# Performance work log

Hardware: AMD Instinct MI355X
Metric: run time of the kernel (lower is better)

## Reference

```python
import jax, jax.numpy as jnp
import numpy as np

N_NODES = 100000


def _gcn_layer(x, src, dst, W, b, n_nodes):
    # x: [N, Cin]; src/dst already include self-loops
    h = x @ W  # [N, Cout]
    deg = jax.ops.segment_sum(jnp.ones_like(dst, dtype=h.dtype), dst,
                              num_segments=n_nodes)  # in-degree incl. self-loop
    dinv = jnp.where(deg > 0, deg ** -0.5, 0.0)
    norm = dinv[src] * dinv[dst]  # [E]
    msg = h[src] * norm[:, None]  # [E, Cout]
    out = jax.ops.segment_sum(msg, dst, num_segments=n_nodes)
    return out + b


def setup_inputs() -> dict:
    key = jax.random.key(0)
    k1, k2, k3, k4, k5, k6, k7 = jax.random.split(key, 7)
    E = 6400000
    x = jax.random.normal(k1, (N_NODES, 5), dtype=jnp.float32)
    edge_index = jax.random.randint(k2, (2, E), 0, N_NODES, dtype=jnp.int64)
    edge_f = jax.random.normal(k3, (E,), dtype=jnp.float32)
    edge_attr = jax.random.normal(k4, (E, 1), dtype=jnp.float32)
    # GCNConv params (glorot-ish scale)
    W1 = jax.random.normal(k5, (5, 8), dtype=jnp.float32) * (1.0 / np.sqrt(5))
    b1 = jnp.zeros((8,), dtype=jnp.float32)
    W2 = jax.random.normal(k6, (8, 5), dtype=jnp.float32) * (1.0 / np.sqrt(8))
    b2 = jnp.zeros((5,), dtype=jnp.float32)
    return {"x": x, "edge_index": edge_index, "edge_f": edge_f,
            "edge_attr": edge_attr, "W1": W1, "b1": b1, "W2": W2, "b2": b2}


def reference(x, edge_index, edge_f, edge_attr, W1, b1, W2, b2):
    n = x.shape[0]
    loops = jnp.arange(n, dtype=edge_index.dtype)
    src = jnp.concatenate([edge_index[0], loops])  # add self-loops (PyG default)
    dst = jnp.concatenate([edge_index[1], loops])
    h = _gcn_layer(x, src, dst, W1, b1, n)
    h = _gcn_layer(h, src, dst, W2, b2, n)
    return h
```

## Files before the change

### kernel.cpp

```cpp
#include <hip/hip_runtime.h>
#include <hip/hip_fp16.h>


#define TPB 256
#define VPB 256
#define B_BITS 8
#define MAXB 512
#define CAP 17408
#define NBLK_E 512
#define EPB 12500
#define SCT 512
#define DGT 512

typedef int int4e __attribute__((ext_vector_type(4)));
typedef _Float16 h8 __attribute__((ext_vector_type(8)));

__device__ __forceinline__ int4e ntload4(const int* p) {
    return __builtin_nontemporal_load((const int4e*)p);
}
__device__ __forceinline__ int ntload(const int* p) {
    return __builtin_nontemporal_load(p);
}

__global__ void k_init(int B, int* __restrict__ bpos) {
    int b = blockIdx.x * blockDim.x + threadIdx.x;
    if (b < B) bpos[b] = b * CAP;
}

__global__ __launch_bounds__(SCT) void k_scat(const int* __restrict__ src,
        const int* __restrict__ dst, int E, int B,
        int* __restrict__ bpos, int* __restrict__ pairs) {
    __shared__ int sorted[EPB];
    __shared__ int hist[MAXB], scn[MAXB], cur[MAXB], gbase[MAXB];
    int t = threadIdx.x;
    for (int i = t; i < MAXB; i += SCT) hist[i] = 0;
    __syncthreads();
    int lo = blockIdx.x * EPB;
    int n = min(E - lo, EPB);
    int n4 = n & ~3;
    for (int i = t * 4; i < n4; i += SCT * 4) {
        int4e d4 = ntload4(dst + lo + i);
        atomicAdd(&hist[d4.x >> B_BITS], 1);
        atomicAdd(&hist[d4.y >> B_BITS], 1);
        atomicAdd(&hist[d4.z >> B_BITS], 1);
        atomicAdd(&hist[d4.w >> B_BITS], 1);
    }
    for (int i = n4 + t; i < n; i += SCT)
        atomicAdd(&hist[dst[lo + i] >> B_BITS], 1);
    __syncthreads();
    if (t < MAXB) scn[t] = hist[t];
    __syncthreads();
    for (int off = 1; off < MAXB; off <<= 1) {
        int v = (t >= off && t < MAXB) ? scn[t - off] : 0;
        __syncthreads();
        if (t < MAXB) scn[t] += v;
        __syncthreads();
    }
    if (t < MAXB) {
        int h = hist[t];
        cur[t] = scn[t] - h;
        gbase[t] = (t < B && h) ? atomicAdd(&bpos[t], h) : 0;
    }
    __syncthreads();
    for (int i = t * 4; i < n4; i += SCT * 4) {
        int4e d4 = ntload4(dst + lo + i);
        int4e s4 = ntload4(src + lo + i);
        int p;
        p = atomicAdd(&cur[d4.x >> B_BITS], 1); sorted[p] = (s4.x << B_BITS) | (d4.x & (VPB - 1));
        p = atomicAdd(&cur[d4.y >> B_BITS], 1); sorted[p] = (s4.y << B_BITS) | (d4.y & (VPB - 1));
        p = atomicAdd(&cur[d4.z >> B_BITS], 1); sorted[p] = (s4.z << B_BITS) | (d4.z & (VPB - 1));
        p = atomicAdd(&cur[d4.w >> B_BITS], 1); sorted[p] = (s4.w << B_BITS) | (d4.w & (VPB - 1));
    }
    for (int i = n4 + t; i < n; i += SCT) {
        int d = dst[lo + i], s = src[lo + i];
        int p = atomicAdd(&cur[d >> B_BITS], 1);
        sorted[p] = (s << B_BITS) | (d & (VPB - 1));
    }
    __syncthreads();
    int wave = t >> 6, lane = t & 63;
    for (int b2 = wave; b2 < B; b2 += (SCT >> 6)) {
        int h = hist[b2];
        int st = scn[b2] - h;
        int gb = gbase[b2];
        for (int j = lane; j < h; j += 64)
            pairs[gb + j] = sorted[st + j];
    }
}

__global__ __launch_bounds__(DGT) void k_degxs(const int* __restrict__ pairs,
        const int* __restrict__ bpos, int N,
        const float* __restrict__ x,
        unsigned int* __restrict__ jinfo, _Float16* __restrict__ xs) {
    __shared__ int hist[VPB];
    __shared__ int scn[VPB];
    int t = threadIdx.x, b = blockIdx.x;
    if (t < VPB) hist[t] = 0;
    __syncthreads();
    int base = b * CAP;
    int n = bpos[b] - base, n4 = n & ~3;
    for (int i = t * 4; i < n4; i += DGT * 4) {
        int4e p = ntload4(pairs + base + i);
        atomicAdd(&hist[p.x & (VPB - 1)], 1);
        atomicAdd(&hist[p.y & (VPB - 1)], 1);
        atomicAdd(&hist[p.z & (VPB - 1)], 1);
        atomicAdd(&hist[p.w & (VPB - 1)], 1);
    }
    for (int i = n4 + t; i < n; i += DGT)
        atomicAdd(&hist[pairs[base + i] & (VPB - 1)], 1);
    __syncthreads();
    if (t < VPB) scn[t] = hist[t];
    __syncthreads();
    for (int off = 1; off < VPB; off <<= 1) {
        int v = (t >= off && t < VPB) ? scn[t - off] : 0;
        __syncthreads();
        if (t < VPB) scn[t] += v;
        __syncthreads();
    }
    int node = b * VPB + t;
    if (t < VPB && node < N) {
        int h = hist[t];
        int start = base + scn[t] - h;
        jinfo[node] = ((unsigned int)start << 9) | (unsigned int)h;
        float di = rsqrtf((float)(h + 1));
        const float* xp = x + (size_t)node * 5;
        h8 v;
        v[0] = (_Float16)(xp[0] * di); v[1] = (_Float16)(xp[1] * di);
        v[2] = (_Float16)(xp[2] * di); v[3] = (_Float16)(xp[3] * di);
        v[4] = (_Float16)(xp[4] * di);
        v[5] = (_Float16)0.f; v[6] = (_Float16)0.f; v[7] = (_Float16)0.f;
        *(h8*)(xs + (size_t)node * 8) = v;
    }
}

__global__ __launch_bounds__(1024) void k_agg1(const int* __restrict__ pairs_,
        const int* __restrict__ bpos, const unsigned int* __restrict__ jinfo,
        const _Float16* __restrict__ xs, const float* __restrict__ b1,
        const float* __restrict__ W1, const float* __restrict__ W2,
        _Float16* __restrict__ h2s, int N) {
    __shared__ int csr[CAP];
    __shared__ int js[VPB], ct[VPB], cur[VPB];
    int* pairs = (int*)pairs_;
    int t = threadIdx.x, b = blockIdx.x;
    int base = b * CAP;
    if (t < VPB) {
        int node = b * VPB + t;
        int s = 0, c = 0;
        if (node < N) {
            unsigned int u = jinfo[node];
            s = (int)(u >> 9) - base;
            c = (int)(u & 511u);
        }
        js[t] = s; ct[t] = c; cur[t] = s;
    }
    __syncthreads();
    int n = bpos[b] - base, n4 = n & ~3;
    for (int i = t * 4; i < n4; i += 1024 * 4) {
        int4e p = ntload4(pairs + base + i);
        int q;
        q = atomicAdd(&cur[p.x & (VPB - 1)], 1); csr[q] = p.x >> B_BITS;
        q = atomicAdd(&cur[p.y & (VPB - 1)], 1); csr[q] = p.y >> B_BITS;
        q = atomicAdd(&cur[p.z & (VPB - 1)], 1); csr[q] = p.z >> B_BITS;
        q = atomicAdd(&cur[p.w & (VPB - 1)], 1); csr[q] = p.w >> B_BITS;
    }
    for (int i = n4 + t; i < n; i += 1024) {
        int p = pairs[base + i];
        int q = atomicAdd(&cur[p & (VPB - 1)], 1);
        csr[q] = p >> B_BITS;
    }
    __syncthreads();
    for (int i = t; i < n; i += 1024)
        __builtin_nontemporal_store(csr[i], pairs + base + i);
    int lane = t & 3, ln = t >> 2;
    int node = b * VPB + ln;
    if (node >= N) return;
    int s0 = js[ln], cn = ct[ln];
    float a0 = 0.f, a1 = 0.f, a2 = 0.f, a3 = 0.f, a4 = 0.f;
    int j = lane;
    for (; j + 12 < cn; j += 16) {
        int sA = csr[s0 + j];
        int sB = csr[s0 + j + 4];
        int sC = csr[s0 + j + 8];
        int sD = csr[s0 + j + 12];
        h8 vA = *(const h8*)(xs + (size_t)sA * 8);
        h8 vB = *(const h8*)(xs + (size_t)sB * 8);
        h8 vC = *(const h8*)(xs + (size_t)sC * 8);
        h8 vD = *(const h8*)(xs + (size_t)sD * 8);
        a0 += (float)vA[0] + (float)vB[0] + (float)vC[0] + (float)vD[0];
        a1 += (float)vA[1] + (float)vB[1] + (float)vC[1] + (float)vD[1];
        a2 += (float)vA[2] + (float)vB[2] + (float)vC[2] + (float)vD[2];
        a3 += (float)vA[3] + (float)vB[3] + (float)vC[3] + (float)vD[3];
        a4 += (float)vA[4] + (float)vB[4] + (float)vC[4] + (float)vD[4];
    }
    for (; j < cn; j += 4) {
        int sA = csr[s0 + j];
        h8 vA = *(const h8*)(xs + (size_t)sA * 8);
        a0 += (float)vA[0]; a1 += (float)vA[1]; a2 += (float)vA[2];
        a3 += (float)vA[3]; a4 += (float)vA[4];
    }
#pragma unroll
    for (int d = 1; d < 4; d <<= 1) {
        a0 += __shfl_xor(a0, d); a1 += __shfl_xor(a1, d);
        a2 += __shfl_xor(a2, d); a3 += __shfl_xor(a3, d);
        a4 += __shfl_xor(a4, d);
    }
    h8 sv = *(const h8*)(xs + (size_t)node * 8);
    float tc[5];
    tc[0] = a0 + (float)sv[0]; tc[1] = a1 + (float)sv[1];
    tc[2] = a2 + (float)sv[2]; tc[3] = a3 + (float)sv[3];
    tc[4] = a4 + (float)sv[4];
    float di = rsqrtf((float)(cn + 1));
    float o1[8];
#pragma unroll
    for (int jj = 0; jj < 8; ++jj) {
        float h = 0.f;
#pragma unroll
        for (int c = 0; c < 5; ++c) h += tc[c] * W1[c * 8 + jj];
        o1[jj] = h * di + b1[jj];
    }
    if (lane == 0) {
        float hv[5];
#pragma unroll
        for (int k = 0; k < 5; ++k) {
            float h = 0.f;
#pragma unroll
            for (int jj = 0; jj < 8; ++jj) h += o1[jj] * W2[jj * 5 + k];
            hv[k] = h * di;
        }
        h8 w;
        w[0] = (_Float16)hv[0]; w[1] = (_Float16)hv[1]; w[2] = (_Float16)hv[2];
        w[3] = (_Float16)hv[3]; w[4] = (_Float16)hv[4];
        w[5] = (_Float16)0.f; w[6] = (_Float16)0.f; w[7] = (_Float16)0.f;
        *(h8*)(h2s + (size_t)node * 8) = w;
    }
}

__global__ __launch_bounds__(TPB) void k_agg2(const int* __restrict__ pairs,
        const unsigned int* __restrict__ jinfo, const _Float16* __restrict__ h2s,
        const float* __restrict__ b2, float* __restrict__ out, int N) {
    int gid = blockIdx.x * blockDim.x + threadIdx.x;
    int node = gid >> 3, lane = gid & 7;
    if (node >= N) return;
    unsigned int u = jinfo[node];
    int jsa = (int)(u >> 9), cn = (int)(u & 511u);
    float a0 = 0.f, a1 = 0.f, a2 = 0.f, a3 = 0.f, a4 = 0.f;
    int j = lane;
    for (; j + 24 < cn; j += 32) {
        int sA = ntload(pairs + jsa + j);
        int sB = ntload(pairs + jsa + j + 8);
        int sC = ntload(pairs + jsa + j + 16);
        int sD = ntload(pairs + jsa + j + 24);
        h8 vA = *(const h8*)(h2s + (size_t)sA * 8);
        h8 vB = *(const h8*)(h2s + (size_t)sB * 8);
        h8 vC = *(const h8*)(h2s + (size_t)sC * 8);
        h8 vD = *(const h8*)(h2s + (size_t)sD * 8);
        a0 += (float)vA[0] + (float)vB[0] + (float)vC[0] + (float)vD[0];
        a1 += (float)vA[1] + (float)vB[1] + (float)vC[1] + (float)vD[1];
        a2 += (float)vA[2] + (float)vB[2] + (float)vC[2] + (float)vD[2];
        a3 += (float)vA[3] + (float)vB[3] + (float)vC[3] + (float)vD[3];
        a4 += (float)vA[4] + (float)vB[4] + (float)vC[4] + (float)vD[4];
    }
    for (; j < cn; j += 8) {
        int sA = ntload(pairs + jsa + j);
        h8 vA = *(const h8*)(h2s + (size_t)sA * 8);
        a0 += (float)vA[0]; a1 += (float)vA[1]; a2 += (float)vA[2];
        a3 += (float)vA[3]; a4 += (float)vA[4];
    }
#pragma unroll
    for (int d = 1; d < 8; d <<= 1) {
        a0 += __shfl_xor(a0, d); a1 += __shfl_xor(a1, d);
        a2 += __shfl_xor(a2, d); a3 += __shfl_xor(a3, d);
        a4 += __shfl_xor(a4, d);
    }
    if (lane == 0) {
        float di = rsqrtf((float)(cn + 1));
        h8 sv = *(const h8*)(h2s + (size_t)node * 8);
        float* op = out + (size_t)node * 5;
        op[0] = (a0 + (float)sv[0]) * di + b2[0];
        op[1] = (a1 + (float)sv[1]) * di + b2[1];
        op[2] = (a2 + (float)sv[2]) * di + b2[2];
        op[3] = (a3 + (float)sv[3]) * di + b2[3];
        op[4] = (a4 + (float)sv[4]) * di + b2[4];
    }
}

extern "C" void kernel_launch(void* const* d_in, const int* in_sizes, int n_in,
                              void* d_out, int out_size, void* d_ws, size_t ws_size,
                              hipStream_t stream) {
    const float* x   = (const float*)d_in[0];
    const int*  eidx = (const int*)d_in[1];
    const float* W1 = (const float*)d_in[4];
    const float* b1 = (const float*)d_in[5];
    const float* W2 = (const float*)d_in[6];
    const float* b2 = (const float*)d_in[7];
    float* out = (float*)d_out;

    const int N = in_sizes[0] / 5;
    const int E = in_sizes[1] / 2;
    const int* src = eidx;
    const int* dst = eidx + E;

    const int B = (N + VPB - 1) / VPB;

    int*      pairs = (int*)d_ws;
    _Float16* xs    = (_Float16*)(pairs + (size_t)B * CAP);
    _Float16* h2s   = xs + (size_t)8 * N;
    unsigned int* jinfo = (unsigned int*)(h2s + (size_t)8 * N);
    int*      bpos  = (int*)(jinfo + N);

    const int g8N = (8 * N + TPB - 1) / TPB;

    k_init <<<(B + TPB - 1) / TPB, TPB, 0, stream>>>(B, bpos);
    k_scat <<<NBLK_E, SCT, 0, stream>>>(src, dst, E, B, bpos, pairs);
    k_degxs<<<B, DGT, 0, stream>>>(pairs, bpos, N, x, jinfo, xs);
    k_agg1 <<<B, 1024, 0, stream>>>(pairs, bpos, jinfo, xs, b1, W1, W2, h2s, N);
    k_agg2 <<<g8N, TPB, 0, stream>>>(pairs, jinfo, h2s, b2, out, N);
}
```

Baseline: 244.1 us.

## Replace per-node CSR build with shared-memory atomic bucket aggregation

Drops the in-bucket CSR construction and per-node gather. Both aggregation passes now stream the bucketed (src,dst) pairs and accumulate into shared-memory float accumulators with LDS atomics. In-degree is now counted by global atomics during the scatter pass, bucket size is halved to 128 nodes, and the scatter block grows to 1024 threads. This removes the histogram/scan/CSR rewrite passes, at the cost of heavy LDS float-atomic contention and global atomic traffic on the degree array.

New measurement: 815.1 us. 3.34x slower.

```diff
diff --git a/kernel.cpp b/kernel.cpp
--- a/kernel.cpp
+++ b/kernel.cpp
@@ -3,14 +3,14 @@
 
 
 #define TPB 256
-#define VPB 256
-#define B_BITS 8
-#define MAXB 512
-#define CAP 17408
+#define VPB 128
+#define B_BITS 7
+#define MAXB 1024
+#define CAP 8832
 #define NBLK_E 512
 #define EPB 12500
-#define SCT 512
-#define DGT 512
+#define SCT 1024
+#define AGT 512
 
 typedef int int4e __attribute__((ext_vector_type(4)));
 typedef _Float16 h8 __attribute__((ext_vector_type(8)));
@@ -18,18 +18,16 @@
 __device__ __forceinline__ int4e ntload4(const int* p) {
     return __builtin_nontemporal_load((const int4e*)p);
 }
-__device__ __forceinline__ int ntload(const int* p) {
-    return __builtin_nontemporal_load(p);
-}
-
-__global__ void k_init(int B, int* __restrict__ bpos) {
-    int b = blockIdx.x * blockDim.x + threadIdx.x;
-    if (b < B) bpos[b] = b * CAP;
+
+__global__ void k_init(int B, int N, int* __restrict__ bpos, int* __restrict__ deg) {
+    int i = blockIdx.x * blockDim.x + threadIdx.x;
+    if (i < B) bpos[i] = i * CAP;
+    if (i < N) deg[i] = 0;
 }
 
 __global__ __launch_bounds__(SCT) void k_scat(const int* __restrict__ src,
         const int* __restrict__ dst, int E, int B,
-        int* __restrict__ bpos, int* __restrict__ pairs) {
+        int* __restrict__ bpos, int* __restrict__ pairs, int* __restrict__ deg) {
     __shared__ int sorted[EPB];
     __shared__ int hist[MAXB], scn[MAXB], cur[MAXB], gbase[MAXB];
     int t = threadIdx.x;
@@ -40,13 +38,15 @@
     int n4 = n & ~3;
     for (int i = t * 4; i < n4; i += SCT * 4) {
         int4e d4 = ntload4(dst + lo + i);
-        atomicAdd(&hist[d4.x >> B_BITS], 1);
-        atomicAdd(&hist[d4.y >> B_BITS], 1);
-        atomicAdd(&hist[d4.z >> B_BITS], 1);
-        atomicAdd(&hist[d4.w >> B_BITS], 1);
-    }
-    for (int i = n4 + t; i < n; i += SCT)
-        atomicAdd(&hist[dst[lo + i] >> B_BITS], 1);
+        atomicAdd(&hist[d4.x >> B_BITS], 1); atomicAdd(&deg[d4.x], 1);
+        atomicAdd(&hist[d4.y >> B_BITS], 1); atomicAdd(&deg[d4.y], 1);
+        atomicAdd(&hist[d4.z >> B_BITS], 1); atomicAdd(&deg[d4.z], 1);
+        atomicAdd(&hist[d4.w >> B_BITS], 1); atomicAdd(&deg[d4.w], 1);
+    }
+    for (int i = n4 + t; i < n; i += SCT) {
+        int d = dst[lo + i];
+        atomicAdd(&hist[d >> B_BITS], 1); atomicAdd(&deg[d], 1);
+    }
     __syncthreads();
     if (t < MAXB) scn[t] = hist[t];
     __syncthreads();
@@ -78,208 +78,156 @@
     }
     __syncthreads();
     int wave = t >> 6, lane = t & 63;
-    for (int b2 = wave; b2 < B; b2 += (SCT >> 6)) {
-        int h = hist[b2];
-        int st = scn[b2] - h;
-        int gb = gbase[b2];
+    for (int bb = wave; bb < B; bb += (SCT >> 6)) {
+        int h = hist[bb];
+        int st = scn[bb] - h;
+        int gb = gbase[bb];
         for (int j = lane; j < h; j += 64)
             pairs[gb + j] = sorted[st + j];
     }
 }
 
-__global__ __launch_bounds__(DGT) void k_degxs(const int* __restrict__ pairs,
-        const int* __restrict__ bpos, int N,
-        const float* __restrict__ x,
-        unsigned int* __restrict__ jinfo, _Float16* __restrict__ xs) {
-    __shared__ int hist[VPB];
-    __shared__ int scn[VPB];
+__global__ void k_xs(const float* __restrict__ x, const int* __restrict__ deg,
+                     int N, _Float16* __restrict__ xs) {
+    int i = blockIdx.x * blockDim.x + threadIdx.x;
+    if (i >= N) return;
+    float di = rsqrtf((float)(deg[i] + 1));
+    const float* xp = x + (size_t)i * 5;
+    h8 v;
+    v[0] = (_Float16)(xp[0] * di); v[1] = (_Float16)(xp[1] * di);
+    v[2] = (_Float16)(xp[2] * di); v[3] = (_Float16)(xp[3] * di);
+    v[4] = (_Float16)(xp[4] * di);
+    v[5] = (_Float16)0.f; v[6] = (_Float16)0.f; v[7] = (_Float16)0.f;
+    *(h8*)(xs + (size_t)i * 8) = v;
+}
+
+__global__ __launch_bounds__(AGT) void k_agg1(const int* __restrict__ pairs,
+        const int* __restrict__ bpos, const int* __restrict__ deg,
+        const _Float16* __restrict__ xs, const float* __restrict__ W1,
+        const float* __restrict__ b1, const float* __restrict__ W2,
+        _Float16* __restrict__ h2s, int N) {
+    __shared__ float acc[5 * VPB];
     int t = threadIdx.x, b = blockIdx.x;
-    if (t < VPB) hist[t] = 0;
+    for (int i = t; i < 5 * VPB; i += AGT) acc[i] = 0.f;
     __syncthreads();
     int base = b * CAP;
     int n = bpos[b] - base, n4 = n & ~3;
-    for (int i = t * 4; i < n4; i += DGT * 4) {
+    for (int i = t * 4; i < n4; i += AGT * 4) {
         int4e p = ntload4(pairs + base + i);
-        atomicAdd(&hist[p.x & (VPB - 1)], 1);
-        atomicAdd(&hist[p.y & (VPB - 1)], 1);
-        atomicAdd(&hist[p.z & (VPB - 1)], 1);
-        atomicAdd(&hist[p.w & (VPB - 1)], 1);
-    }
-    for (int i = n4 + t; i < n; i += DGT)
-        atomicAdd(&hist[pairs[base + i] & (VPB - 1)], 1);
-    __syncthreads();
-    if (t < VPB) scn[t] = hist[t];
-    __syncthreads();
-    for (int off = 1; off < VPB; off <<= 1) {
-        int v = (t >= off && t < VPB) ? scn[t - off] : 0;
-        __syncthreads();
-        if (t < VPB) scn[t] += v;
-        __syncthreads();
-    }
-    int node = b * VPB + t;
-    if (t < VPB && node < N) {
-        int h = hist[t];
-        int start = base + scn[t] - h;
-        jinfo[node] = ((unsigned int)start << 9) | (unsigned int)h;
-        float di = rsqrtf((float)(h + 1));
-        const float* xp = x + (size_t)node * 5;
-        h8 v;
-        v[0] = (_Float16)(xp[0] * di); v[1] = (_Float16)(xp[1] * di);
-        v[2] = (_Float16)(xp[2] * di); v[3] = (_Float16)(xp[3] * di);
-        v[4] = (_Float16)(xp[4] * di);
-        v[5] = (_Float16)0.f; v[6] = (_Float16)0.f; v[7] = (_Float16)0.f;
-        *(h8*)(xs + (size_t)node * 8) = v;
-    }
-}
-
-__global__ __launch_bounds__(1024) void k_agg1(const int* __restrict__ pairs_,
-        const int* __restrict__ bpos, const unsigned int* __restrict__ jinfo,
-        const _Float16* __restrict__ xs, const float* __restrict__ b1,
-        const float* __restrict__ W1, const float* __restrict__ W2,
-        _Float16* __restrict__ h2s, int N) {
-    __shared__ int csr[CAP];
-    __shared__ int js[VPB], ct[VPB], cur[VPB];
-    int* pairs = (int*)pairs_;
-    int t = threadIdx.x, b = blockIdx.x;
-    int base = b * CAP;
+        int s0 = p.x >> B_BITS, l0 = p.x & (VPB - 1);
+        int s1 = p.y >> B_BITS, l1 = p.y & (VPB - 1);
+        int s2 = p.z >> B_BITS, l2 = p.z & (VPB - 1);
+        int s3 = p.w >> B_BITS, l3 = p.w & (VPB - 1);
+        h8 vA = *(const h8*)(xs + (size_t)s0 * 8);
+        h8 vB = *(const h8*)(xs + (size_t)s1 * 8);
+        h8 vC = *(const h8*)(xs + (size_t)s2 * 8);
+        h8 vD = *(const h8*)(xs + (size_t)s3 * 8);
+        atomicAdd(&acc[l0], (float)vA[0]); atomicAdd(&acc[l0 + VPB], (float)vA[1]);
+        atomicAdd(&acc[l0 + 2 * VPB], (float)vA[2]); atomicAdd(&acc[l0 + 3 * VPB], (float)vA[3]);
+        atomicAdd(&acc[l0 + 4 * VPB], (float)vA[4]);
+        atomicAdd(&acc[l1], (float)vB[0]); atomicAdd(&acc[l1 + VPB], (float)vB[1]);
+        atomicAdd(&acc[l1 + 2 * VPB], (float)vB[2]); atomicAdd(&acc[l1 + 3 * VPB], (float)vB[3]);
+        atomicAdd(&acc[l1 + 4 * VPB], (float)vB[4]);
+        atomicAdd(&acc[l2], (float)vC[0]); atomicAdd(&acc[l2 + VPB], (float)vC[1]);
+        atomicAdd(&acc[l2 + 2 * VPB], (float)vC[2]); atomicAdd(&acc[l2 + 3 * VPB], (float)vC[3]);
+        atomicAdd(&acc[l2 + 4 * VPB], (float)vC[4]);
+        atomicAdd(&acc[l3], (float)vD[0]); atomicAdd(&acc[l3 + VPB], (float)vD[1]);
+        atomicAdd(&acc[l3 + 2 * VPB], (float)vD[2]); atomicAdd(&acc[l3 + 3 * VPB], (float)vD[3]);
+        atomicAdd(&acc[l3 + 4 * VPB], (float)vD[4]);
+    }
+    for (int i = n4 + t; i < n; i += AGT) {
+        int p = pairs[base + i];
+        int s = p >> B_BITS, l = p & (VPB - 1);
+        h8 v = *(const h8*)(xs + (size_t)s * 8);
+        atomicAdd(&acc[l], (float)v[0]); atomicAdd(&acc[l + VPB], (float)v[1]);
+        atomicAdd(&acc[l + 2 * VPB], (float)v[2]); atomicAdd(&acc[l + 3 * VPB], (float)v[3]);
+        atomicAdd(&acc[l + 4 * VPB], (float)v[4]);
+    }
+    __syncthreads();
     if (t < VPB) {
         int node = b * VPB + t;
-        int s = 0, c = 0;
         if (node < N) {
-            unsigned int u = jinfo[node];
-            s = (int)(u >> 9) - base;
-            c = (int)(u & 511u);
+            float di = rsqrtf((float)(deg[node] + 1));
+            h8 sv = *(const h8*)(xs + (size_t)node * 8);
+            float tc[5];
+#pragma unroll
+            for (int c = 0; c < 5; ++c) tc[c] = acc[t + c * VPB] + (float)sv[c];
+            float o1[8];
+#pragma unroll
+            for (int jj = 0; jj < 8; ++jj) {
+                float h = 0.f;
+#pragma unroll
+                for (int c = 0; c < 5; ++c) h += tc[c] * W1[c * 8 + jj];
+                o1[jj] = h * di + b1[jj];
+            }
+            h8 w;
+#pragma unroll
+            for (int k = 0; k < 5; ++k) {
+                float h = 0.f;
+#pragma unroll
+                for (int jj = 0; jj < 8; ++jj) h += o1[jj] * W2[jj * 5 + k];
+                w[k] = (_Float16)(h * di);
+            }
+            w[5] = (_Float16)0.f; w[6] = (_Float16)0.f; w[7] = (_Float16)0.f;
+            *(h8*)(h2s + (size_t)node * 8) = w;
         }
-        js[t] = s; ct[t] = c; cur[t] = s;
-    }
-    __syncthreads();
+    }
+}
+
+__global__ __launch_bounds__(AGT) void k_agg2(const int* __restrict__ pairs,
+        const int* __restrict__ bpos, const int* __restrict__ deg,
+        const _Float16* __restrict__ h2s, const float* __restrict__ b2,
+        float* __restrict__ out, int N) {
+    __shared__ float acc[5 * VPB];
+    int t = threadIdx.x, b = blockIdx.x;
+    for (int i = t; i < 5 * VPB; i += AGT) acc[i] = 0.f;
+    __syncthreads();
+    int base = b * CAP;
     int n = bpos[b] - base, n4 = n & ~3;
-    for (int i = t * 4; i < n4; i += 1024 * 4) {
+    for (int i = t * 4; i < n4; i += AGT * 4) {
         int4e p = ntload4(pairs + base + i);
-        int q;
-        q = atomicAdd(&cur[p.x & (VPB - 1)], 1); csr[q] = p.x >> B_BITS;
-        q = atomicAdd(&cur[p.y & (VPB - 1)], 1); csr[q] = p.y >> B_BITS;
-        q = atomicAdd(&cur[p.z & (VPB - 1)], 1); csr[q] = p.z >> B_BITS;
-        q = atomicAdd(&cur[p.w & (VPB - 1)], 1); csr[q] = p.w >> B_BITS;
-    }
-    for (int i = n4 + t; i < n; i += 1024) {
+        int s0 = p.x >> B_BITS, l0 = p.x & (VPB - 1);
+        int s1 = p.y >> B_BITS, l1 = p.y & (VPB - 1);
+        int s2 = p.z >> B_BITS, l2 = p.z & (VPB - 1);
+        int s3 = p.w >> B_BITS, l3 = p.w & (VPB - 1);
+        h8 vA = *(const h8*)(h2s + (size_t)s0 * 8);
+        h8 vB = *(const h8*)(h2s + (size_t)s1 * 8);
+        h8 vC = *(const h8*)(h2s + (size_t)s2 * 8);
+        h8 vD = *(const h8*)(h2s + (size_t)s3 * 8);
+        atomicAdd(&acc[l0], (float)vA[0]); atomicAdd(&acc[l0 + VPB], (float)vA[1]);
+        atomicAdd(&acc[l0 + 2 * VPB], (float)vA[2]); atomicAdd(&acc[l0 + 3 * VPB], (float)vA[3]);
+        atomicAdd(&acc[l0 + 4 * VPB], (float)vA[4]);
+        atomicAdd(&acc[l1], (float)vB[0]); atomicAdd(&acc[l1 + VPB], (float)vB[1]);
+        atomicAdd(&acc[l1 + 2 * VPB], (float)vB[2]); atomicAdd(&acc[l1 + 3 * VPB], (float)vB[3]);
+        atomicAdd(&acc[l1 + 4 * VPB], (float)vB[4]);
+        atomicAdd(&acc[l2], (float)vC[0]); atomicAdd(&acc[l2 + VPB], (float)vC[1]);
+        atomicAdd(&acc[l2 + 2 * VPB], (float)vC[2]); atomicAdd(&acc[l2 + 3 * VPB], (float)vC[3]);
+        atomicAdd(&acc[l2 + 4 * VPB], (float)vC[4]);
+        atomicAdd(&acc[l3], (float)vD[0]); atomicAdd(&acc[l3 + VPB], (float)vD[1]);
+        atomicAdd(&acc[l3 + 2 * VPB], (float)vD[2]); atomicAdd(&acc[l3 + 3 * VPB], (float)vD[3]);
+        atomicAdd(&acc[l3 + 4 * VPB], (float)vD[4]);
+    }
+    for (int i = n4 + t; i < n; i += AGT) {
         int p = pairs[base + i];
-        int q = atomicAdd(&cur[p & (VPB - 1)], 1);
-        csr[q] = p >> B_BITS;
-    }
-    __syncthreads();
-    for (int i = t; i < n; i += 1024)
-        __builtin_nontemporal_store(csr[i], pairs + base + i);
-    int lane = t & 3, ln = t >> 2;
-    int node = b * VPB + ln;
-    if (node >= N) return;
-    int s0 = js[ln], cn = ct[ln];
-    float a0 = 0.f, a1 = 0.f, a2 = 0.f, a3 = 0.f, a4 = 0.f;
-    int j = lane;
-    for (; j + 12 < cn; j += 16) {
-        int sA = csr[s0 + j];
-        int sB = csr[s0 + j + 4];
-        int sC = csr[s0 + j + 8];
-        int sD = csr[s0 + j + 12];
-        h8 vA = *(const h8*)(xs + (size_t)sA * 8);
-        h8 vB = *(const h8*)(xs + (size_t)sB * 8);
-        h8 vC = *(const h8*)(xs + (size_t)sC * 8);
-        h8 vD = *(const h8*)(xs + (size_t)sD * 8);
-        a0 += (float)vA[0] + (float)vB[0] + (float)vC[0] + (float)vD[0];
-        a1 += (float)vA[1] + (float)vB[1] + (float)vC[1] + (float)vD[1];
-        a2 += (float)vA[2] + (float)vB[2] + (float)vC[2] + (float)vD[2];
-        a3 += (float)vA[3] + (float)vB[3] + (float)vC[3] + (float)vD[3];
-        a4 += (float)vA[4] + (float)vB[4] + (float)vC[4] + (float)vD[4];
-    }
-    for (; j < cn; j += 4) {
-        int sA = csr[s0 + j];
-        h8 vA = *(const h8*)(xs + (size_t)sA * 8);
-        a0 += (float)vA[0]; a1 += (float)vA[1]; a2 += (float)vA[2];
-        a3 += (float)vA[3]; a4 += (float)vA[4];
-    }
-#pragma unroll
-    for (int d = 1; d < 4; d <<= 1) {
-        a0 += __shfl_xor(a0, d); a1 += __shfl_xor(a1, d);
-        a2 += __shfl_xor(a2, d); a3 += __shfl_xor(a3, d);
-        a4 += __shfl_xor(a4, d);
-    }
-    h8 sv = *(const h8*)(xs + (size_t)node * 8);
-    float tc[5];
-    tc[0] = a0 + (float)sv[0]; tc[1] = a1 + (float)sv[1];
-    tc[2] = a2 + (float)sv[2]; tc[3] = a3 + (float)sv[3];
-    tc[4] = a4 + (float)sv[4];
-    float di = rsqrtf((float)(cn + 1));
-    float o1[8];
-#pragma unroll
-    for (int jj = 0; jj < 8; ++jj) {
-        float h = 0.f;
-#pragma unroll
-        for (int c = 0; c < 5; ++c) h += tc[c] * W1[c * 8 + jj];
-        o1[jj] = h * di + b1[jj];
-    }
-    if (lane == 0) {
-        float hv[5];
-#pragma unroll
-        for (int k = 0; k < 5; ++k) {
-            float h = 0.f;
-#pragma unroll
-            for (int jj = 0; jj < 8; ++jj) h += o1[jj] * W2[jj * 5 + k];
-            hv[k] = h * di;
+        int s = p >> B_BITS, l = p & (VPB - 1);
+        h8 v = *(const h8*)(h2s + (size_t)s * 8);
+        atomicAdd(&acc[l], (float)v[0]); atomicAdd(&acc[l + VPB], (float)v[1]);
+        atomicAdd(&acc[l + 2 * VPB], (float)v[2]); atomicAdd(&acc[l + 3 * VPB], (float)v[3]);
+        atomicAdd(&acc[l + 4 * VPB], (float)v[4]);
+    }
+    __syncthreads();
+    if (t < VPB) {
+        int node = b * VPB + t;
+        if (node < N) {
+            float di = rsqrtf((float)(deg[node] + 1));
+            h8 sv = *(const h8*)(h2s + (size_t)node * 8);
+            float* op = out + (size_t)node * 5;
+            op[0] = (acc[t] + (float)sv[0]) * di + b2[0];
+            op[1] = (acc[t + VPB] + (float)sv[1]) * di + b2[1];
+            op[2] = (acc[t + 2 * VPB] + (float)sv[2]) * di + b2[2];
+            op[3] = (acc[t + 3 * VPB] + (float)sv[3]) * di + b2[3];
+            op[4] = (acc[t + 4 * VPB] + (float)sv[4]) * di + b2[4];
         }
-        h8 w;
-        w[0] = (_Float16)hv[0]; w[1] = (_Float16)hv[1]; w[2] = (_Float16)hv[2];
-        w[3] = (_Float16)hv[3]; w[4] = (_Float16)hv[4];
-        w[5] = (_Float16)0.f; w[6] = (_Float16)0.f; w[7] = (_Float16)0.f;
-        *(h8*)(h2s + (size_t)node * 8) = w;
-    }
-}
-
-__global__ __launch_bounds__(TPB) void k_agg2(const int* __restrict__ pairs,
-        const unsigned int* __restrict__ jinfo, const _Float16* __restrict__ h2s,
-        const float* __restrict__ b2, float* __restrict__ out, int N) {
-    int gid = blockIdx.x * blockDim.x + threadIdx.x;
-    int node = gid >> 3, lane = gid & 7;
-    if (node >= N) return;
-    unsigned int u = jinfo[node];
-    int jsa = (int)(u >> 9), cn = (int)(u & 511u);
-    float a0 = 0.f, a1 = 0.f, a2 = 0.f, a3 = 0.f, a4 = 0.f;
-    int j = lane;
-    for (; j + 24 < cn; j += 32) {
-        int sA = ntload(pairs + jsa + j);
-        int sB = ntload(pairs + jsa + j + 8);
-        int sC = ntload(pairs + jsa + j + 16);
-        int sD = ntload(pairs + jsa + j + 24);
-        h8 vA = *(const h8*)(h2s + (size_t)sA * 8);
-        h8 vB = *(const h8*)(h2s + (size_t)sB * 8);
-        h8 vC = *(const h8*)(h2s + (size_t)sC * 8);
-        h8 vD = *(const h8*)(h2s + (size_t)sD * 8);
-        a0 += (float)vA[0] + (float)vB[0] + (float)vC[0] + (float)vD[0];
-        a1 += (float)vA[1] + (float)vB[1] + (float)vC[1] + (float)vD[1];
-        a2 += (float)vA[2] + (float)vB[2] + (float)vC[2] + (float)vD[2];
-        a3 += (float)vA[3] + (float)vB[3] + (float)vC[3] + (float)vD[3];
-        a4 += (float)vA[4] + (float)vB[4] + (float)vC[4] + (float)vD[4];
-    }
-    for (; j < cn; j += 8) {
-        int sA = ntload(pairs + jsa + j);
-        h8 vA = *(const h8*)(h2s + (size_t)sA * 8);
-        a0 += (float)vA[0]; a1 += (float)vA[1]; a2 += (float)vA[2];
-        a3 += (float)vA[3]; a4 += (float)vA[4];
-    }
-#pragma unroll
-    for (int d = 1; d < 8; d <<= 1) {
-        a0 += __shfl_xor(a0, d); a1 += __shfl_xor(a1, d);
-        a2 += __shfl_xor(a2, d); a3 += __shfl_xor(a3, d);
-        a4 += __shfl_xor(a4, d);
-    }
-    if (lane == 0) {
-        float di = rsqrtf((float)(cn + 1));
-        h8 sv = *(const h8*)(h2s + (size_t)node * 8);
-        float* op = out + (size_t)node * 5;
-        op[0] = (a0 + (float)sv[0]) * di + b2[0];
-        op[1] = (a1 + (float)sv[1]) * di + b2[1];
-        op[2] = (a2 + (float)sv[2]) * di + b2[2];
-        op[3] = (a3 + (float)sv[3]) * di + b2[3];
-        op[4] = (a4 + (float)sv[4]) * di + b2[4];
     }
 }
 
@@ -304,14 +252,14 @@
     int*      pairs = (int*)d_ws;
     _Float16* xs    = (_Float16*)(pairs + (size_t)B * CAP);
     _Float16* h2s   = xs + (size_t)8 * N;
-    unsigned int* jinfo = (unsigned int*)(h2s + (size_t)8 * N);
-    int*      bpos  = (int*)(jinfo + N);
-
-    const int g8N = (8 * N + TPB - 1) / TPB;
-
-    k_init <<<(B + TPB - 1) / TPB, TPB, 0, stream>>>(B, bpos);
-    k_scat <<<NBLK_E, SCT, 0, stream>>>(src, dst, E, B, bpos, pairs);
-    k_degxs<<<B, DGT, 0, stream>>>(pairs, bpos, N, x, jinfo, xs);
-    k_agg1 <<<B, 1024, 0, stream>>>(pairs, bpos, jinfo, xs, b1, W1, W2, h2s, N);
-    k_agg2 <<<g8N, TPB, 0, stream>>>(pairs, jinfo, h2s, b2, out, N);
-}
+    int*      deg   = (int*)(h2s + (size_t)8 * N);
+    int*      bpos  = deg + N;
+
+    const int gN = (N + TPB - 1) / TPB;
+
+    k_init <<<gN, TPB, 0, stream>>>(B, N, bpos, deg);
+    k_scat <<<NBLK_E, SCT, 0, stream>>>(src, dst, E, B, bpos, pairs, deg);
+    k_xs   <<<gN, TPB, 0, stream>>>(x, deg, N, xs);
+    k_agg1 <<<B, AGT, 0, stream>>>(pairs, bpos, deg, xs, W1, b1, W2, h2s, N);
+    k_agg2 <<<B, AGT, 0, stream>>>(pairs, bpos, deg, h2s, b2, out, N);
+}
```

## Merge degree and CSR build into one kernel, split layer-1 gather out

Applied to the files above, without the earlier changes.

The degree histogram, xs scaling and the in-block counting sort to CSR move into a single 1024-thread kernel, k_pre. This removes the separate k_degxs pass, which re-read the pairs buffer. The layer-1 gather becomes its own fine-grained kernel with 8 lanes per node, reading CSR indices from global memory instead of LDS. The aim is better occupancy and load balance for the gather, since the old version was limited by the 68KB LDS footprint. The cost is an extra global read of the sorted indices.

After: 255.4 us. +4.6%, slower.

```diff
diff --git a/kernel.cpp b/kernel.cpp
--- a/kernel.cpp
+++ b/kernel.cpp
@@ -10,7 +10,6 @@
 #define NBLK_E 512
 #define EPB 12500
 #define SCT 512
-#define DGT 512
 
 typedef int int4e __attribute__((ext_vector_type(4)));
 typedef _Float16 h8 __attribute__((ext_vector_type(8)));
@@ -78,34 +77,34 @@
     }
     __syncthreads();
     int wave = t >> 6, lane = t & 63;
-    for (int b2 = wave; b2 < B; b2 += (SCT >> 6)) {
-        int h = hist[b2];
-        int st = scn[b2] - h;
-        int gb = gbase[b2];
+    for (int bb = wave; bb < B; bb += (SCT >> 6)) {
+        int h = hist[bb];
+        int st = scn[bb] - h;
+        int gb = gbase[bb];
         for (int j = lane; j < h; j += 64)
             pairs[gb + j] = sorted[st + j];
     }
 }
 
-__global__ __launch_bounds__(DGT) void k_degxs(const int* __restrict__ pairs,
-        const int* __restrict__ bpos, int N,
-        const float* __restrict__ x,
-        unsigned int* __restrict__ jinfo, _Float16* __restrict__ xs) {
-    __shared__ int hist[VPB];
+__global__ __launch_bounds__(1024) void k_pre(int* __restrict__ pairs,
+        const int* __restrict__ bpos, const float* __restrict__ x,
+        unsigned int* __restrict__ jinfo, _Float16* __restrict__ xs, int N) {
+    __shared__ int csr[CAP];
+    __shared__ int hist[VPB], cur[VPB];
     __shared__ int scn[VPB];
     int t = threadIdx.x, b = blockIdx.x;
     if (t < VPB) hist[t] = 0;
     __syncthreads();
     int base = b * CAP;
     int n = bpos[b] - base, n4 = n & ~3;
-    for (int i = t * 4; i < n4; i += DGT * 4) {
+    for (int i = t * 4; i < n4; i += 1024 * 4) {
         int4e p = ntload4(pairs + base + i);
         atomicAdd(&hist[p.x & (VPB - 1)], 1);
         atomicAdd(&hist[p.y & (VPB - 1)], 1);
         atomicAdd(&hist[p.z & (VPB - 1)], 1);
         atomicAdd(&hist[p.w & (VPB - 1)], 1);
     }
-    for (int i = n4 + t; i < n; i += DGT)
+    for (int i = n4 + t; i < n; i += 1024)
         atomicAdd(&hist[pairs[base + i] & (VPB - 1)], 1);
     __syncthreads();
     if (t < VPB) scn[t] = hist[t];
@@ -117,43 +116,23 @@
         __syncthreads();
     }
     int node = b * VPB + t;
-    if (t < VPB && node < N) {
+    if (t < VPB) {
         int h = hist[t];
-        int start = base + scn[t] - h;
-        jinfo[node] = ((unsigned int)start << 9) | (unsigned int)h;
-        float di = rsqrtf((float)(h + 1));
-        const float* xp = x + (size_t)node * 5;
-        h8 v;
-        v[0] = (_Float16)(xp[0] * di); v[1] = (_Float16)(xp[1] * di);
-        v[2] = (_Float16)(xp[2] * di); v[3] = (_Float16)(xp[3] * di);
-        v[4] = (_Float16)(xp[4] * di);
-        v[5] = (_Float16)0.f; v[6] = (_Float16)0.f; v[7] = (_Float16)0.f;
-        *(h8*)(xs + (size_t)node * 8) = v;
-    }
-}
-
-__global__ __launch_bounds__(1024) void k_agg1(const int* __restrict__ pairs_,
-        const int* __restrict__ bpos, const unsigned int* __restrict__ jinfo,
-        const _Float16* __restrict__ xs, const float* __restrict__ b1,
-        const float* __restrict__ W1, const float* __restrict__ W2,
-        _Float16* __restrict__ h2s, int N) {
-    __shared__ int csr[CAP];
-    __shared__ int js[VPB], ct[VPB], cur[VPB];
-    int* pairs = (int*)pairs_;
-    int t = threadIdx.x, b = blockIdx.x;
-    int base = b * CAP;
-    if (t < VPB) {
-        int node = b * VPB + t;
-        int s = 0, c = 0;
+        int sl = scn[t] - h;
+        cur[t] = sl;
         if (node < N) {
-            unsigned int u = jinfo[node];
-            s = (int)(u >> 9) - base;
-            c = (int)(u & 511u);
+            jinfo[node] = ((unsigned int)(base + sl) << 9) | (unsigned int)h;
+            float di = rsqrtf((float)(h + 1));
+            const float* xp = x + (size_t)node * 5;
+            h8 v;
+            v[0] = (_Float16)(xp[0] * di); v[1] = (_Float16)(xp[1] * di);
+            v[2] = (_Float16)(xp[2] * di); v[3] = (_Float16)(xp[3] * di);
+            v[4] = (_Float16)(xp[4] * di);
+            v[5] = (_Float16)0.f; v[6] = (_Float16)0.f; v[7] = (_Float16)0.f;
+            *(h8*)(xs + (size_t)node * 8) = v;
         }
-        js[t] = s; ct[t] = c; cur[t] = s;
-    }
-    __syncthreads();
-    int n = bpos[b] - base, n4 = n & ~3;
+    }
+    __syncthreads();
     for (int i = t * 4; i < n4; i += 1024 * 4) {
         int4e p = ntload4(pairs + base + i);
         int q;
@@ -170,17 +149,24 @@
     __syncthreads();
     for (int i = t; i < n; i += 1024)
         __builtin_nontemporal_store(csr[i], pairs + base + i);
-    int lane = t & 3, ln = t >> 2;
-    int node = b * VPB + ln;
+}
+
+__global__ __launch_bounds__(TPB) void k_g1(const int* __restrict__ pairs,
+        const unsigned int* __restrict__ jinfo, const _Float16* __restrict__ xs,
+        const float* __restrict__ W1, const float* __restrict__ b1,
+        const float* __restrict__ W2, _Float16* __restrict__ h2s, int N) {
+    int gid = blockIdx.x * blockDim.x + threadIdx.x;
+    int node = gid >> 3, lane = gid & 7;
     if (node >= N) return;
-    int s0 = js[ln], cn = ct[ln];
+    unsigned int u = jinfo[node];
+    int jsa = (int)(u >> 9), cn = (int)(u & 511u);
     float a0 = 0.f, a1 = 0.f, a2 = 0.f, a3 = 0.f, a4 = 0.f;
     int j = lane;
-    for (; j + 12 < cn; j += 16) {
-        int sA = csr[s0 + j];
-        int sB = csr[s0 + j + 4];
-        int sC = csr[s0 + j + 8];
-        int sD = csr[s0 + j + 12];
+    for (; j + 24 < cn; j += 32) {
+        int sA = ntload(pairs + jsa + j);
+        int sB = ntload(pairs + jsa + j + 8);
+        int sC = ntload(pairs + jsa + j + 16);
+        int sD = ntload(pairs + jsa + j + 24);
         h8 vA = *(const h8*)(xs + (size_t)sA * 8);
         h8 vB = *(const h8*)(xs + (size_t)sB * 8);
         h8 vC = *(const h8*)(xs + (size_t)sC * 8);
@@ -191,24 +177,24 @@
         a3 += (float)vA[3] + (float)vB[3] + (float)vC[3] + (float)vD[3];
         a4 += (float)vA[4] + (float)vB[4] + (float)vC[4] + (float)vD[4];
     }
-    for (; j < cn; j += 4) {
-        int sA = csr[s0 + j];
+    for (; j < cn; j += 8) {
+        int sA = ntload(pairs + jsa + j);
         h8 vA = *(const h8*)(xs + (size_t)sA * 8);
         a0 += (float)vA[0]; a1 += (float)vA[1]; a2 += (float)vA[2];
         a3 += (float)vA[3]; a4 += (float)vA[4];
     }
 #pragma unroll
-    for (int d = 1; d < 4; d <<= 1) {
+    for (int d = 1; d < 8; d <<= 1) {
         a0 += __shfl_xor(a0, d); a1 += __shfl_xor(a1, d);
         a2 += __shfl_xor(a2, d); a3 += __shfl_xor(a3, d);
         a4 += __shfl_xor(a4, d);
     }
+    float di = rsqrtf((float)(cn + 1));
     h8 sv = *(const h8*)(xs + (size_t)node * 8);
     float tc[5];
     tc[0] = a0 + (float)sv[0]; tc[1] = a1 + (float)sv[1];
     tc[2] = a2 + (float)sv[2]; tc[3] = a3 + (float)sv[3];
     tc[4] = a4 + (float)sv[4];
-    float di = rsqrtf((float)(cn + 1));
     float o1[8];
 #pragma unroll
     for (int jj = 0; jj < 8; ++jj) {
@@ -218,23 +204,20 @@
         o1[jj] = h * di + b1[jj];
     }
     if (lane == 0) {
-        float hv[5];
+        h8 w;
 #pragma unroll
         for (int k = 0; k < 5; ++k) {
             float h = 0.f;
 #pragma unroll
             for (int jj = 0; jj < 8; ++jj) h += o1[jj] * W2[jj * 5 + k];
-            hv[k] = h * di;
+            w[k] = (_Float16)(h * di);
         }
-        h8 w;
-        w[0] = (_Float16)hv[0]; w[1] = (_Float16)hv[1]; w[2] = (_Float16)hv[2];
-        w[3] = (_Float16)hv[3]; w[4] = (_Float16)hv[4];
         w[5] = (_Float16)0.f; w[6] = (_Float16)0.f; w[7] = (_Float16)0.f;
         *(h8*)(h2s + (size_t)node * 8) = w;
     }
 }
 
-__global__ __launch_bounds__(TPB) void k_agg2(const int* __restrict__ pairs,
+__global__ __launch_bounds__(TPB) void k_g2(const int* __restrict__ pairs,
         const unsigned int* __restrict__ jinfo, const _Float16* __restrict__ h2s,
         const float* __restrict__ b2, float* __restrict__ out, int N) {
     int gid = blockIdx.x * blockDim.x + threadIdx.x;
@@ -311,7 +294,7 @@
 
     k_init <<<(B + TPB - 1) / TPB, TPB, 0, stream>>>(B, bpos);
     k_scat <<<NBLK_E, SCT, 0, stream>>>(src, dst, E, B, bpos, pairs);
-    k_degxs<<<B, DGT, 0, stream>>>(pairs, bpos, N, x, jinfo, xs);
-    k_agg1 <<<B, 1024, 0, stream>>>(pairs, bpos, jinfo, xs, b1, W1, W2, h2s, N);
-    k_agg2 <<<g8N, TPB, 0, stream>>>(pairs, jinfo, h2s, b2, out, N);
-}
+    k_pre  <<<B, 1024, 0, stream>>>(pairs, bpos, x, jinfo, xs, N);
+    k_g1   <<<g8N, TPB, 0, stream>>>(pairs, jinfo, xs, W1, b1, W2, h2s, N);
+    k_g2   <<<g8N, TPB, 0, stream>>>(pairs, jinfo, h2s, b2, out, N);
+}
```
